# Kernel optimization log

Hardware: AMD Instinct MI355X
Metric: run time of the kernel (lower is better)

The kernel has to match this reference:

```python
import jax, jax.numpy as jnp
import numpy as np

B, T, D, R = 4, 1024, 512, 64
SLOTS = (1024, 256, 64)
K = 16


def _layernorm(x, g, b, eps=1e-5):
    m = jnp.mean(x, axis=-1, keepdims=True)
    v = jnp.mean(jnp.square(x - m), axis=-1, keepdims=True)
    return (x - m) * jax.lax.rsqrt(v + eps) * g + b


def _signed_softmax(x):
    # signed softmax over the slot axis: sign(x) * softmax(|x|)
    return jnp.sign(x) * jax.nn.softmax(jnp.abs(x), axis=-1)


def _transition_delta(src_val, src_state, dst_val, W, k, n_dst):
    # Low-rank bilinear routing: logits [B, Ns, Nd]
    q = jnp.einsum('bsd,dr->bsr', src_val, W[0])
    kk = jnp.einsum('bnd,dr->bnr', dst_val, W[1])
    logits = jnp.einsum('bsr,bnr->bsn', q, kk) / jnp.sqrt(jnp.float32(W.shape[-1]))
    v, idx = jax.lax.top_k(logits, k)                      # [B, Ns, k]
    w = jnp.sign(v) * jax.nn.softmax(jnp.abs(v), axis=-1)  # signed_abs_softmax over selected edges
    c = w * jax.nn.softplus(src_state)[:, :, None]         # state-weighted edge coefficients [B, Ns, k]
    d = src_val.shape[-1]
    edge_val = (c[..., None] * src_val[:, :, None, :]).reshape(src_val.shape[0], -1, d)
    idx_f = idx.reshape(idx.shape[0], -1)
    cf = c.reshape(c.shape[0], -1)

    def _scatter(i, ev, cc):
        dv = jnp.zeros((n_dst, d), src_val.dtype).at[i].add(ev)
        ds = jnp.zeros((n_dst,), src_val.dtype).at[i].add(cc)
        return ds, dv

    return jax.vmap(_scatter)(idx_f, edge_val, cf)


def _apply_delta(state, val, dstate, dval, g, b):
    # residual merge, then constrain: signed softmax state + LayerNorm values
    return _signed_softmax(state + dstate), _layernorm(val + dval, g, b)


def setup_inputs() -> dict:
    key = jax.random.key(0)
    ks = jax.random.split(key, 20)
    rn = lambda k, s, sc=1.0: jax.random.normal(k, s, jnp.float32) * sc
    return {
        'tok_val': rn(ks[0], (B, T, D)),
        'tok_state': rn(ks[1], (B, T)),
        'mem_state0': rn(ks[2], (B, SLOTS[0]), 0.02),
        'mem_val0': rn(ks[3], (B, SLOTS[0], D), 0.02),
        'mem_state1': rn(ks[4], (B, SLOTS[1]), 0.02),
        'mem_val1': rn(ks[5], (B, SLOTS[1], D), 0.02),
        'mem_state2': rn(ks[6], (B, SLOTS[2]), 0.02),
        'mem_val2': rn(ks[7], (B, SLOTS[2], D), 0.02),
        'write_route': rn(ks[8], (1, 2, D, R), 0.05),
        'prop_route': rn(ks[9], (3, 2, D, R), 0.05),
        'level_route': rn(ks[10], (2, 2, D, R), 0.05),
        'skip_route': rn(ks[11], (2, 2, D, R), 0.05),
        'skip_gates': jnp.full((2,), -1.5, jnp.float32),
        'ln_gamma': jnp.ones((3, D), jnp.float32),
        'ln_beta': jnp.zeros((3, D), jnp.float32),
        'read_route': rn(ks[12], (3, 2, D, R), 0.05),
        'read_proj': rn(ks[13], (3, D, D), 0.02),
        'read_gates': jnp.zeros((3,), jnp.float32),
        'topk': K,
    }


def reference(tok_val, tok_state, mem_state0, mem_val0, mem_state1, mem_val1,
              mem_state2, mem_val2, write_route, prop_route, level_route,
              skip_route, skip_gates, ln_gamma, ln_beta, read_route, read_proj,
              read_gates, topk):
    k = int(topk)
    S0, S1, S2 = mem_state0.shape[1], mem_state1.shape[1], mem_state2.shape[1]

    # --- level 0: token write + pairwise propagation ---
    ds, dv = _transition_delta(tok_val, tok_state, mem_val0, write_route[0], min(k, S0), S0)
    s0, v0 = _apply_delta(mem_state0, mem_val0, ds, dv, ln_gamma[0], ln_beta[0])
    ds, dv = _transition_delta(v0, s0, v0, prop_route[0], min(k, S0), S0)
    s0, v0 = _apply_delta(s0, v0, ds, dv, ln_gamma[0], ln_beta[0])

    # --- level 1: transition from level 0, gated skip from tokens, propagation ---
    ds, dv = _transition_delta(v0, s0, mem_val1, level_route[0], min(k, S1), S1)
    s1, v1 = _apply_delta(mem_state1, mem_val1, ds, dv, ln_gamma[1], ln_beta[1])
    g = jax.nn.sigmoid(skip_gates[0])
    ds, dv = _transition_delta(tok_val, tok_state, v1, skip_route[0], min(k, S1), S1)
    s1, v1 = _apply_delta(s1, v1, g * ds, g * dv, ln_gamma[1], ln_beta[1])
    ds, dv = _transition_delta(v1, s1, v1, prop_route[1], min(k, S1), S1)
    s1, v1 = _apply_delta(s1, v1, ds, dv, ln_gamma[1], ln_beta[1])

    # --- level 2: transition from level 1, gated skip from level 0, propagation ---
    ds, dv = _transition_delta(v1, s1, mem_val2, level_route[1], min(k, S2), S2)
    s2, v2 = _apply_delta(mem_state2, mem_val2, ds, dv, ln_gamma[2], ln_beta[2])
    g = jax.nn.sigmoid(skip_gates[1])
    ds, dv = _transition_delta(v0, s0, v2, skip_route[1], min(k, S2), S2)
    s2, v2 = _apply_delta(s2, v2, g * ds, g * dv, ln_gamma[2], ln_beta[2])
    ds, dv = _transition_delta(v2, s2, v2, prop_route[2], min(k, S2), S2)
    s2, v2 = _apply_delta(s2, v2, ds, dv, ln_gamma[2], ln_beta[2])

    # --- read: tokens attend over each memory level, gated projected residual ---
    out = tok_val
    for l, mv in enumerate((v0, v1, v2)):
        q = jnp.einsum('btd,dr->btr', tok_val, read_route[l, 0])
        kk = jnp.einsum('bnd,dr->bnr', mv, read_route[l, 1])
        logits = jnp.einsum('btr,bnr->btn', q, kk) / jnp.sqrt(jnp.float32(R))
        attn = jax.nn.softmax(logits, axis=-1)
        r = jnp.einsum('btn,bnd->btd', attn, mv)
        out = out + jax.nn.sigmoid(read_gates[l]) * jnp.einsum('btd,de->bte', r, read_proj[l])
    return out
```

## Files before the change

kernel.cpp:

```cpp
#include <hip/hip_runtime.h>
#include <math.h>

typedef __attribute__((ext_vector_type(8))) short short8;
typedef __attribute__((ext_vector_type(4))) float floatx4;

static __device__ __forceinline__ short f2bf(float f) {
    union { float f; unsigned u; } c; c.f = f;
    unsigned r = c.u + 0x7FFF + ((c.u >> 16) & 1);
    return (short)(r >> 16);
}

__launch_bounds__(256)
__global__ void gemm_f32_nt_kernel(const float* __restrict__ A, const float* __restrict__ B,
                                   float* __restrict__ C, int M, int N, int K,
                                   long sA, long sB, long sC, float alpha)
{
    __shared__ float As[32][68];
    __shared__ float Bs[32][68];
    const float* Ab = A + (long)blockIdx.z * sA;
    const float* Bb = B + (long)blockIdx.z * sB;
    float* Cb = C + (long)blockIdx.z * sC;
    int m0 = blockIdx.x * 64, n0 = blockIdx.y * 64;
    int t = threadIdx.x;
    int tx = t & 15, ty = t >> 4;
    float acc[4][4] = {};

    for (int k0 = 0; k0 < K; k0 += 32) {
        {
            int m = t >> 3;
            int kk = (t & 7) * 4;
#pragma unroll
            for (int h = 0; h < 2; ++h) {
                float4 v = *(const float4*)&Ab[(long)(m0 + m + 32 * h) * K + k0 + kk];
                As[kk + 0][m + 32 * h] = v.x; As[kk + 1][m + 32 * h] = v.y;
                As[kk + 2][m + 32 * h] = v.z; As[kk + 3][m + 32 * h] = v.w;
            }
        }
        {
            int n = t >> 3;
            int kk = (t & 7) * 4;
#pragma unroll
            for (int h = 0; h < 2; ++h) {
                float4 v = *(const float4*)&Bb[(long)(n0 + n + 32 * h) * K + k0 + kk];
                Bs[kk + 0][n + 32 * h] = v.x; Bs[kk + 1][n + 32 * h] = v.y;
                Bs[kk + 2][n + 32 * h] = v.z; Bs[kk + 3][n + 32 * h] = v.w;
            }
        }
        __syncthreads();
#pragma unroll 4
        for (int k = 0; k < 32; ++k) {
            float4 a = *(const float4*)&As[k][ty * 4];
            float4 b = *(const float4*)&Bs[k][tx * 4];
            float av[4] = { a.x, a.y, a.z, a.w };
            float bv[4] = { b.x, b.y, b.z, b.w };
#pragma unroll
            for (int i = 0; i < 4; ++i)
#pragma unroll
                for (int j = 0; j < 4; ++j) acc[i][j] += av[i] * bv[j];
        }
        __syncthreads();
    }
#pragma unroll
    for (int i = 0; i < 4; ++i) {
        float4 r;
        r.x = alpha * acc[i][0]; r.y = alpha * acc[i][1];
        r.z = alpha * acc[i][2]; r.w = alpha * acc[i][3];
        *(float4*)&Cb[(long)(m0 + ty * 4 + i) * N + n0 + tx * 4] = r;
    }
}

__launch_bounds__(256)
__global__ void proj_splitk_kernel(const float* __restrict__ Aq, const float* __restrict__ Ak,
                                   const float* __restrict__ Wq, const float* __restrict__ Wk,
                                   float* __restrict__ part,
                                   int Mq, int Mk, long sAq, long sAk, int Bn)
{
    __shared__ float As[32][68];
    __shared__ float Bs[32][68];
    int mqT = Mq >> 6;
    int xt = blockIdx.x, s = blockIdx.y, b = blockIdx.z;
    const float* A; const float* W; int row0, orow;
    if (xt < mqT) { A = Aq + (long)b * sAq; W = Wq; row0 = xt * 64; orow = row0; }
    else { A = Ak + (long)b * sAk; W = Wk; row0 = (xt - mqT) * 64; orow = Mq + row0; }
    int t = threadIdx.x, tx = t & 15, ty = t >> 4;
    float acc[4][4] = {};
    int kbase = s * 64;

    for (int k0 = kbase; k0 < kbase + 64; k0 += 32) {
        {
            int m = t >> 3;
            int kk = (t & 7) * 4;
#pragma unroll
            for (int h = 0; h < 2; ++h) {
                float4 v = *(const float4*)&A[(long)(row0 + m + 32 * h) * 512 + k0 + kk];
                As[kk + 0][m + 32 * h] = v.x; As[kk + 1][m + 32 * h] = v.y;
                As[kk + 2][m + 32 * h] = v.z; As[kk + 3][m + 32 * h] = v.w;
            }
        }
        {
            int kk = t >> 3;
            int nn = (t & 7) * 8;
            float4 v0 = *(const float4*)&W[(long)(k0 + kk) * 64 + nn];
            float4 v1 = *(const float4*)&W[(long)(k0 + kk) * 64 + nn + 4];
            *(float4*)&Bs[kk][nn] = v0;
            *(float4*)&Bs[kk][nn + 4] = v1;
        }
        __syncthreads();
#pragma unroll 4
        for (int k = 0; k < 32; ++k) {
            float4 a = *(const float4*)&As[k][ty * 4];
            float4 b2 = *(const float4*)&Bs[k][tx * 4];
            float av[4] = { a.x, a.y, a.z, a.w };
            float bv[4] = { b2.x, b2.y, b2.z, b2.w };
#pragma unroll
            for (int i = 0; i < 4; ++i)
#pragma unroll
                for (int j = 0; j < 4; ++j) acc[i][j] += av[i] * bv[j];
        }
        __syncthreads();
    }
    long base = ((long)(s * Bn + b) * (Mq + Mk) + orow) * 64;
#pragma unroll
    for (int i = 0; i < 4; ++i)
        *(float4*)&part[base + (long)(ty * 4 + i) * 64 + tx * 4] =
            make_float4(acc[i][0], acc[i][1], acc[i][2], acc[i][3]);
}

__launch_bounds__(256)
__global__ void proj_reduce_kernel(const float* __restrict__ part,
                                   float* __restrict__ qout, float* __restrict__ kout,
                                   int Mq, int Mk, int Bn)
{
    int idx = blockIdx.x * 256 + threadIdx.x;
    int size4b = (Mq + Mk) * 16;
    int total4 = Bn * size4b;
    if (idx >= total4) return;
    const float4* p4 = (const float4*)part;
    long stride4 = (long)total4;
    float4 s = p4[idx];
#pragma unroll
    for (int ss = 1; ss < 8; ++ss) {
        float4 v = p4[ss * stride4 + idx];
        s.x += v.x; s.y += v.y; s.z += v.z; s.w += v.w;
    }
    int b = idx / size4b;
    int rem = idx - b * size4b;
    int r = rem >> 4;
    int c4 = rem & 15;
    if (r < Mq) ((float4*)qout)[((long)b * Mq + r) * 16 + c4] = s;
    else        ((float4*)kout)[((long)b * Mk + (r - Mq)) * 16 + c4] = s;
}

__launch_bounds__(256)
__global__ void gemm_mfma_kernel(const float* __restrict__ A, const unsigned short* __restrict__ Bt,
                                 float* __restrict__ C, int M, int N, int K,
                                 long sA, long sBt, long sC,
                                 float alpha, const float* __restrict__ gate, int gateIdx,
                                 float beta, const float* __restrict__ initC)
{
    __shared__ short As[2048];
    __shared__ short Bs[2048];
    const float* Ab = A + (long)blockIdx.z * sA;
    const unsigned short* Bb = Bt + (long)blockIdx.z * sBt;
    float* Cb = C + (long)blockIdx.z * sC;
    const float* Ib = initC ? initC + (long)blockIdx.z * sC : nullptr;
    int m0 = blockIdx.x * 64, n0 = blockIdx.y * 64;
    int t = threadIdx.x, wave = t >> 6, lane = t & 63;
    int sr = wave * 16 + (lane & 15);
    int sk = (lane >> 4) * 8;
    floatx4 acc[4] = {};

    for (int k0 = 0; k0 < K; k0 += 32) {
        const float* ap = &Ab[(long)(m0 + sr) * K + k0 + sk];
        float4 f0 = *(const float4*)ap;
        float4 f1 = *(const float4*)(ap + 4);
        short8 av;
        av[0] = f2bf(f0.x); av[1] = f2bf(f0.y); av[2] = f2bf(f0.z); av[3] = f2bf(f0.w);
        av[4] = f2bf(f1.x); av[5] = f2bf(f1.y); av[6] = f2bf(f1.z); av[7] = f2bf(f1.w);
        short8 bv = *(const short8*)&Bb[(long)(n0 + sr) * K + k0 + sk];
        ((short8*)As)[t] = av;
        ((short8*)Bs)[t] = bv;
        __syncthreads();
        short8 bf = ((short8*)Bs)[wave * 64 + lane];
#pragma unroll
        for (int mt = 0; mt < 4; ++mt) {
            short8 af = ((short8*)As)[mt * 64 + lane];
            acc[mt] = __builtin_amdgcn_mfma_f32_16x16x32_bf16(af, bf, acc[mt], 0, 0, 0);
        }
        __syncthreads();
    }
    float a = alpha;
    if (gate) a *= 1.f / (1.f + expf(-gate[gateIdx]));
    int col = n0 + wave * 16 + (lane & 15);
#pragma unroll
    for (int mt = 0; mt < 4; ++mt) {
#pragma unroll
        for (int r = 0; r < 4; ++r) {
            int row = m0 + mt * 16 + (lane >> 4) * 4 + r;
            long off = (long)row * N + col;
            float v = a * acc[mt][r];
            if (Ib) v += Ib[off];
            else if (beta != 0.f) v += Cb[off];
            Cb[off] = v;
        }
    }
}

__global__ void transpose_bf16_kernel(const float* __restrict__ in, unsigned short* __restrict__ out,
                                      int Rr, int Cc, long sIn, long sOut)
{
    __shared__ float tile[32][33];
    const float* I = in + (long)blockIdx.z * sIn;
    unsigned short* O = out + (long)blockIdx.z * sOut;
    int c0 = blockIdx.x * 32, r0 = blockIdx.y * 32;
    int tx = threadIdx.x, ty = threadIdx.y;
#pragma unroll
    for (int i = 0; i < 32; i += 8)
        tile[ty + i][tx] = I[(long)(r0 + ty + i) * Cc + c0 + tx];
    __syncthreads();
#pragma unroll
    for (int i = 0; i < 32; i += 8)
        O[(long)(c0 + ty + i) * Rr + r0 + tx] = (unsigned short)f2bf(tile[tx][ty + i]);
}

template<int CNT>
__launch_bounds__(256)
__global__ void topk_coeff_kernel(const float* __restrict__ logits,
                                  const float* __restrict__ state,
                                  int* __restrict__ idx_out, float* __restrict__ c_out,
                                  int* __restrict__ cnt, int nsLog, int Nd)
{
    int wave = threadIdx.x >> 6, lane = threadIdx.x & 63;
    long row = (long)blockIdx.x * 4 + wave;
    const float* L = logits + row * Nd;
    float vreg[CNT];
    if (CNT >= 4) {
#pragma unroll
        for (int q = 0; q < CNT / 4; ++q) {
            float4 v = *(const float4*)&L[lane * CNT + q * 4];
            vreg[q * 4 + 0] = v.x; vreg[q * 4 + 1] = v.y;
            vreg[q * 4 + 2] = v.z; vreg[q * 4 + 3] = v.w;
        }
    } else {
#pragma unroll
        for (int tt = 0; tt < CNT; ++tt) vreg[tt] = L[lane * CNT + tt];
    }

    float m = 0.f, sum = 0.f;
    float myv = 0.f; int myi = 0;
#pragma unroll
    for (int it = 0; it < 16; ++it) {
        float best = -INFINITY; int bidx = 0x7fffffff;
#pragma unroll
        for (int tt = 0; tt < CNT; ++tt) {
            if (vreg[tt] > best) { best = vreg[tt]; bidx = lane * CNT + tt; }
        }
#pragma unroll
        for (int off = 32; off; off >>= 1) {
            float ov = __shfl_down(best, off);
            int   oi = __shfl_down(bidx, off);
            if (ov > best || (ov == best && oi < bidx)) { best = ov; bidx = oi; }
        }
        best = __shfl(best, 0);
        bidx = __shfl(bidx, 0);
        if (it == lane) { myv = best; myi = bidx; }
        float ab = fabsf(best);
        float nm = fmaxf(m, ab);
        sum = sum * expf(m - nm) + expf(ab - nm);
        m = nm;
#pragma unroll
        for (int tt = 0; tt < CNT; ++tt)
            if (lane * CNT + tt == bidx) vreg[tt] = -INFINITY;
    }
    if (lane < 16) {
        float st = state[row];
        float sp = fmaxf(st, 0.f) + log1pf(expf(-fabsf(st)));
        float sgn = (myv > 0.f) ? 1.f : ((myv < 0.f) ? -1.f : 0.f);
        float w = expf(fabsf(myv) - m) / sum;
        c_out[row * 16 + lane] = sgn * w * sp;
        idx_out[row * 16 + lane] = myi;
        int b = (int)(row >> nsLog);
        atomicAdd(&cnt[b * Nd + myi], 1);
    }
}

__launch_bounds__(256)
__global__ void scan_kernel(int* __restrict__ cnt, int* __restrict__ offs, int N)
{
    __shared__ int sums[256];
    int t = threadIdx.x;
    int chunk = N >> 8;
    int base = t * chunk;
    int lc[16];
    int s = 0;
    for (int i = 0; i < chunk; ++i) { lc[i] = cnt[base + i]; s += lc[i]; }
    sums[t] = s;
    __syncthreads();
    for (int off = 1; off < 256; off <<= 1) {
        int v = (t >= off) ? sums[t - off] : 0;
        __syncthreads();
        sums[t] += v;
        __syncthreads();
    }
    int run = sums[t] - s;
    for (int i = 0; i < chunk; ++i) {
        offs[base + i] = run;
        run += lc[i];
        cnt[base + i] = 0;
    }
    if (t == 255) offs[N] = run;
}

__launch_bounds__(256)
__global__ void fill_edges_kernel(const int* __restrict__ idx, const int* __restrict__ offs,
                                  int* __restrict__ cursor, int* __restrict__ elist,
                                  int nsShift, int Nd, int E)
{
    int e = blockIdx.x * 256 + threadIdx.x;
    if (e >= E) return;
    int b = e >> nsShift;
    int d = b * Nd + idx[e];
    int pos = offs[d] + atomicAdd(&cursor[d], 1);
    elist[pos] = e;
}

#define ECHUNK 512
__launch_bounds__(256)
__global__ void gather_ln_kernel(const float* __restrict__ src_val, const float* __restrict__ c,
                                 const int* __restrict__ elist, const int* __restrict__ offs,
                                 const float* __restrict__ v_in, float* __restrict__ v_out,
                                 float* __restrict__ ds, int* __restrict__ cursor,
                                 const float* __restrict__ gamma, const float* __restrict__ beta,
                                 const float* __restrict__ gatePtr, int gateIdx, int nsShift)
{
    __shared__ float sc[ECHUNK];
    __shared__ int   srow[ECHUNK];
    __shared__ float part[4][512];
    __shared__ float pcs[4];
    __shared__ float red[4];
    long row = blockIdx.x;
    int t = threadIdx.x, w = t >> 6, lane = t & 63;
    int e0 = offs[row], e1 = offs[row + 1];
    int mask = (1 << nsShift) - 1;
    int cb = lane * 8;
    float a[8] = {};
    float cs = 0.f;
    float gate = 1.f;
    if (gatePtr) gate = 1.f / (1.f + expf(-gatePtr[gateIdx]));

    for (int cstart = e0; cstart < e1; cstart += ECHUNK) {
        int cnt = min(e1 - cstart, ECHUNK);
        for (int i = t; i < cnt; i += 256) {
            int e = elist[cstart + i];
            sc[i] = c[e];
            int b = e >> nsShift;
            int s = (e & mask) >> 4;
            srow[i] = (b << (nsShift - 4)) + s;
        }
        __syncthreads();
        int j = w;
        for (; j + 12 < cnt; j += 16) {
            float c0 = sc[j], c1 = sc[j + 4], c2 = sc[j + 8], c3 = sc[j + 12];
            const float* p0 = src_val + ((long)srow[j]      << 9) + cb;
            const float* p1 = src_val + ((long)srow[j + 4]  << 9) + cb;
            const float* p2 = src_val + ((long)srow[j + 8]  << 9) + cb;
            const float* p3 = src_val + ((long)srow[j + 12] << 9) + cb;
            float4 x00 = *(const float4*)p0,       x01 = *(const float4*)(p0 + 4);
            float4 x10 = *(const float4*)p1,       x11 = *(const float4*)(p1 + 4);
            float4 x20 = *(const float4*)p2,       x21 = *(const float4*)(p2 + 4);
            float4 x30 = *(const float4*)p3,       x31 = *(const float4*)(p3 + 4);
            a[0] += c0 * x00.x + c1 * x10.x + c2 * x20.x + c3 * x30.x;
            a[1] += c0 * x00.y + c1 * x10.y + c2 * x20.y + c3 * x30.y;
            a[2] += c0 * x00.z + c1 * x10.z + c2 * x20.z + c3 * x30.z;
            a[3] += c0 * x00.w + c1 * x10.w + c2 * x20.w + c3 * x30.w;
            a[4] += c0 * x01.x + c1 * x11.x + c2 * x21.x + c3 * x31.x;
            a[5] += c0 * x01.y + c1 * x11.y + c2 * x21.y + c3 * x31.y;
            a[6] += c0 * x01.z + c1 * x11.z + c2 * x21.z + c3 * x31.z;
            a[7] += c0 * x01.w + c1 * x11.w + c2 * x21.w + c3 * x31.w;
            cs += c0 + c1 + c2 + c3;
        }
        for (; j < cnt; j += 4) {
            float cv = sc[j];
            const float* p = src_val + ((long)srow[j] << 9) + cb;
            float4 x0 = *(const float4*)p, x1 = *(const float4*)(p + 4);
            a[0] += cv * x0.x; a[1] += cv * x0.y; a[2] += cv * x0.z; a[3] += cv * x0.w;
            a[4] += cv * x1.x; a[5] += cv * x1.y; a[6] += cv * x1.z; a[7] += cv * x1.w;
            cs += cv;
        }
        __syncthreads();
    }
#pragma unroll
    for (int i = 0; i < 8; ++i) part[w][cb + i] = a[i];
    if (lane == 0) pcs[w] = cs;
    __syncthreads();
    float r0 = part[0][t] + part[1][t] + part[2][t] + part[3][t];
    float r1 = part[0][t + 256] + part[1][t + 256] + part[2][t + 256] + part[3][t + 256];
    if (t == 0) { ds[row] = pcs[0] + pcs[1] + pcs[2] + pcs[3]; cursor[row] = 0; }

    const float* vi = v_in + (row << 9);
    float x0 = vi[t]       + gate * r0;
    float x1 = vi[t + 256] + gate * r1;
    float s = x0 + x1;
    for (int off = 32; off; off >>= 1) s += __shfl_down(s, off);
    if ((t & 63) == 0) red[t >> 6] = s;
    __syncthreads();
    float mean = (red[0] + red[1] + red[2] + red[3]) * (1.f / 512.f);
    float d0 = x0 - mean, d1 = x1 - mean;
    float ss = d0 * d0 + d1 * d1;
    for (int off = 32; off; off >>= 1) ss += __shfl_down(ss, off);
    __syncthreads();
    if ((t & 63) == 0) red[t >> 6] = ss;
    __syncthreads();
    float var = (red[0] + red[1] + red[2] + red[3]) * (1.f / 512.f);
    float rstd = rsqrtf(var + 1e-5f);
    float* vo = v_out + (row << 9);
    vo[t]       = d0 * rstd * gamma[t]       + beta[t];
    vo[t + 256] = d1 * rstd * gamma[t + 256] + beta[t + 256];
}

__launch_bounds__(256)
__global__ void apply_state_kernel(const float* __restrict__ s_in, const float* __restrict__ ds,
                                   float* __restrict__ s_out, int Nd,
                                   const float* __restrict__ gatePtr, int gateIdx)
{
    __shared__ float sh[1024];
    __shared__ float red[4];
    int b = blockIdx.x, t = threadIdx.x;
    float gate = 1.f;
    if (gatePtr) gate = 1.f / (1.f + expf(-gatePtr[gateIdx]));
    float lmax = 0.f;
    for (int i = t; i < Nd; i += 256) {
        float x = s_in[b * Nd + i] + gate * ds[b * Nd + i];
        sh[i] = x;
        lmax = fmaxf(lmax, fabsf(x));
    }
    for (int off = 32; off; off >>= 1) lmax = fmaxf(lmax, __shfl_down(lmax, off));
    if ((t & 63) == 0) red[t >> 6] = lmax;
    __syncthreads();
    float bmax = fmaxf(fmaxf(red[0], red[1]), fmaxf(red[2], red[3]));
    float lsum = 0.f;
    for (int i = t; i < Nd; i += 256) lsum += expf(fabsf(sh[i]) - bmax);
    for (int off = 32; off; off >>= 1) lsum += __shfl_down(lsum, off);
    __syncthreads();
    if ((t & 63) == 0) red[t >> 6] = lsum;
    __syncthreads();
    float inv = 1.f / (red[0] + red[1] + red[2] + red[3]);
    for (int i = t; i < Nd; i += 256) {
        float x = sh[i];
        float sgn = (x > 0.f) ? 1.f : ((x < 0.f) ? -1.f : 0.f);
        s_out[b * Nd + i] = sgn * expf(fabsf(x) - bmax) * inv;
    }
}

__launch_bounds__(256)
__global__ void softmax_rows_kernel(float* __restrict__ logits, int Nd)
{
    __shared__ float red[4];
    long row = blockIdx.x;
    int t = threadIdx.x;
    float* L = logits + row * (long)Nd;
    float lmax = -INFINITY;
    for (int i = t; i < Nd; i += 256) lmax = fmaxf(lmax, L[i]);
    for (int off = 32; off; off >>= 1) lmax = fmaxf(lmax, __shfl_down(lmax, off));
    if ((t & 63) == 0) red[t >> 6] = lmax;
    __syncthreads();
    float bmax = fmaxf(fmaxf(red[0], red[1]), fmaxf(red[2], red[3]));
    float lsum = 0.f;
    for (int i = t; i < Nd; i += 256) lsum += expf(L[i] - bmax);
    for (int off = 32; off; off >>= 1) lsum += __shfl_down(lsum, off);
    __syncthreads();
    if ((t & 63) == 0) red[t >> 6] = lsum;
    __syncthreads();
    float inv = 1.f / (red[0] + red[1] + red[2] + red[3]);
    for (int i = t; i < Nd; i += 256) L[i] = expf(L[i] - bmax) * inv;
}

extern "C" void kernel_launch(void* const* d_in, const int* in_sizes, int n_in,
                              void* d_out, int out_size, void* d_ws, size_t ws_size,
                              hipStream_t stream)
{
    const int Bn = 4, T = 1024, D = 512, R = 64;
    const int S0 = 1024, S1 = 256, S2 = 64;
    const long RT = (long)D * R;

    const float* tok_val    = (const float*)d_in[0];
    const float* tok_state  = (const float*)d_in[1];
    const float* mem_state0 = (const float*)d_in[2];
    const float* mem_val0   = (const float*)d_in[3];
    const float* mem_state1 = (const float*)d_in[4];
    const float* mem_val1   = (const float*)d_in[5];
    const float* mem_state2 = (const float*)d_in[6];
    const float* mem_val2   = (const float*)d_in[7];
    const float* write_route= (const float*)d_in[8];
    const float* prop_route = (const float*)d_in[9];
    const float* level_route= (const float*)d_in[10];
    const float* skip_route = (const float*)d_in[11];
    const float* skip_gates = (const float*)d_in[12];
    const float* ln_gamma   = (const float*)d_in[13];
    const float* ln_beta    = (const float*)d_in[14];
    const float* read_route = (const float*)d_in[15];
    const float* read_proj  = (const float*)d_in[16];
    const float* read_gates = (const float*)d_in[17];
    float* out = (float*)d_out;

    float* p = (float*)d_ws;
    float* v0  = p; p += (long)Bn * S0 * D;
    float* v0b = p; p += (long)Bn * S0 * D;
    float* s0  = p; p += Bn * S0;
    float* v1  = p; p += (long)Bn * S1 * D;
    float* v1b = p; p += (long)Bn * S1 * D;
    float* s1  = p; p += Bn * S1;
    float* v2  = p; p += (long)Bn * S2 * D;
    float* v2b = p; p += (long)Bn * S2 * D;
    float* s2  = p; p += Bn * S2;
    float* qb  = p; p += (long)Bn * T * R;
    float* kb  = p; p += (long)Bn * S0 * R;
    float* lb  = p; p += (long)Bn * T * S0;
    float* cbuf= p; p += (long)Bn * T * 16;
    int*   ib  = (int*)p; p += (long)Bn * T * 16;
    float* dsb = p; p += Bn * S0;
    float* rb  = p; p += (long)Bn * T * D;
    int* cntb  = (int*)p; p += Bn * S0;
    int* curb  = (int*)p; p += Bn * S0;
    int* offsb = (int*)p; p += Bn * S0 + 1;
    int* elistb= (int*)p; p += (long)Bn * T * 16;
    unsigned short* projT = (unsigned short*)p; p += (3 * (long)D * D) / 2 + 4;
    unsigned short* mvT   = (unsigned short*)p; p += ((long)Bn * D * S0) / 2 + 4;
    float* partb = p; p += 8L * Bn * (T + S0) * R;

    auto proj = [&](const float* Aq, const float* Ak, const float* Wq, const float* Wk,
                    int Mq, int Mk, long sAq, long sAk, float* qout, float* kout) {
        proj_splitk_kernel<<<dim3((Mq + Mk) / 64, 8, Bn), 256, 0, stream>>>(
            Aq, Ak, Wq, Wk, partb, Mq, Mk, sAq, sAk, Bn);
        int total4 = Bn * (Mq + Mk) * 16;
        proj_reduce_kernel<<<(total4 + 255) / 256, 256, 0, stream>>>(
            partb, qout, kout, Mq, Mk, Bn);
    };

    hipMemsetAsync(cntb, 0, (size_t)2 * Bn * S0 * sizeof(int), stream);

    auto trans = [&](const float* sv, const float* ss, const float* dval,
                     const float* W, int Ns, int Nd,
                     const float* v_in, float* v_out, const float* sin, float* sout,
                     int lvl, const float* gptr, int gidx) {
        proj(sv, dval, W, W + RT, Ns, Nd, (long)Ns * D, (long)Nd * D, qb, kb);
        gemm_f32_nt_kernel<<<dim3(Ns / 64, Nd / 64, Bn), 256, 0, stream>>>(
            qb, kb, lb, Ns, Nd, R, (long)Ns * R, (long)Nd * R, (long)Ns * Nd, 0.125f);
        int nsLog = 31 - __builtin_clz((unsigned)Ns);
        int nsShift = nsLog + 4;
        int rowBlocks = Bn * Ns / 4;
        if (Nd == 1024)
            topk_coeff_kernel<16><<<rowBlocks, 256, 0, stream>>>(lb, ss, ib, cbuf, cntb, nsLog, Nd);
        else if (Nd == 256)
            topk_coeff_kernel<4><<<rowBlocks, 256, 0, stream>>>(lb, ss, ib, cbuf, cntb, nsLog, Nd);
        else
            topk_coeff_kernel<1><<<rowBlocks, 256, 0, stream>>>(lb, ss, ib, cbuf, cntb, nsLog, Nd);
        int E = Bn * Ns * 16;
        scan_kernel<<<1, 256, 0, stream>>>(cntb, offsb, Bn * Nd);
        fill_edges_kernel<<<(E + 255) / 256, 256, 0, stream>>>(ib, offsb, curb, elistb,
                                                               nsShift, Nd, E);
        gather_ln_kernel<<<Bn * Nd, 256, 0, stream>>>(sv, cbuf, elistb, offsb,
                                                      v_in, v_out, dsb, curb,
                                                      ln_gamma + lvl * D, ln_beta + lvl * D,
                                                      gptr, gidx, nsShift);
        apply_state_kernel<<<Bn, 256, 0, stream>>>(sin, dsb, sout, Nd, gptr, gidx);
    };

    trans(tok_val, tok_state, mem_val0, write_route, T, S0,
          mem_val0, v0, mem_state0, s0, 0, nullptr, 0);
    trans(v0, s0, v0, prop_route + 0 * 2 * RT, S0, S0,
          v0, v0b, s0, s0, 0, nullptr, 0);

    trans(v0b, s0, mem_val1, level_route + 0 * 2 * RT, S0, S1,
          mem_val1, v1, mem_state1, s1, 1, nullptr, 0);
    trans(tok_val, tok_state, v1, skip_route + 0 * 2 * RT, T, S1,
          v1, v1, s1, s1, 1, skip_gates, 0);
    trans(v1, s1, v1, prop_route + 1 * 2 * RT, S1, S1,
          v1, v1b, s1, s1, 1, nullptr, 0);

    trans(v1b, s1, mem_val2, level_route + 1 * 2 * RT, S1, S2,
          mem_val2, v2, mem_state2, s2, 2, nullptr, 0);
    trans(v0b, s0, v2, skip_route + 1 * 2 * RT, S0, S2,
          v2, v2, s2, s2, 2, skip_gates, 1);
    trans(v2, s2, v2, prop_route + 2 * 2 * RT, S2, S2,
          v2, v2b, s2, s2, 2, nullptr, 0);

    transpose_bf16_kernel<<<dim3(D / 32, D / 32, 3), dim3(32, 8), 0, stream>>>(
        read_proj, projT, D, D, (long)D * D, (long)D * D);
    const float* mvs[3] = { v0b, v1b, v2b };
    const int nds[3] = { S0, S1, S2 };
    for (int l = 0; l < 3; ++l) {
        const float* mv = mvs[l];
        int Nd = nds[l];
        proj(tok_val, mv, read_route + (long)l * 2 * RT, read_route + (long)l * 2 * RT + RT,
             T, Nd, (long)T * D, (long)Nd * D, qb, kb);
        gemm_f32_nt_kernel<<<dim3(T / 64, Nd / 64, Bn), 256, 0, stream>>>(
            qb, kb, lb, T, Nd, R, (long)T * R, (long)Nd * R, (long)T * Nd, 0.125f);
        softmax_rows_kernel<<<Bn * T, 256, 0, stream>>>(lb, Nd);
        transpose_bf16_kernel<<<dim3(D / 32, Nd / 32, Bn), dim3(32, 8), 0, stream>>>(
            mv, mvT, Nd, D, (long)Nd * D, (long)D * Nd);
        gemm_mfma_kernel<<<dim3(T / 64, D / 64, Bn), 256, 0, stream>>>(
            lb, mvT, rb, T, D, Nd, (long)T * Nd, (long)D * Nd, (long)T * D,
            1.f, nullptr, 0, 0.f, nullptr);
        gemm_mfma_kernel<<<dim3(T / 64, D / 64, Bn), 256, 0, stream>>>(
            rb, projT + (long)l * D * D, out, T, D, D,
            (long)T * D, 0, (long)T * D, 1.f, read_gates, l,
            1.f, (l == 0) ? tok_val : nullptr);
    }
}
```

Baseline: 925.0 us.

## Batch read-side projections and transposes, fuse state update into gather-LN kernel

Generalizes the split-K projection kernel to take a descriptor of up to six segments. All six read-path Q/K projections now run in one launch plus one reduce, and the reduce writes a contiguous layout instead of scattering into separate q/k buffers. The three memory-value transposes are merged into one launch. The state scatter-add and signed softmax now run as extra blocks of the gather-LN kernel using shared-memory atomics, which removes the separate apply-state launch and the global ds buffer. The goal is fewer kernel launches and less tail time, at the cost of branchy segment lookup and atomic accumulation whose order is nondeterministic.

Result: slower. 1.014 ms (+9.6%).

```diff
diff --git a/kernel.cpp b/kernel.cpp
--- a/kernel.cpp
+++ b/kernel.cpp
@@ -69,19 +69,27 @@
     }
 }
 
-__launch_bounds__(256)
-__global__ void proj_splitk_kernel(const float* __restrict__ Aq, const float* __restrict__ Ak,
-                                   const float* __restrict__ Wq, const float* __restrict__ Wk,
-                                   float* __restrict__ part,
-                                   int Mq, int Mk, long sAq, long sAk, int Bn)
+struct ProjDesc {
+    const float* A[6];
+    const float* W[6];
+    long  sA[6];
+    int   tileOff[7];
+    int   rowOff[6];
+    int   Mtot;
+};
+
+__launch_bounds__(256)
+__global__ void proj_splitk_kernel(ProjDesc d, float* __restrict__ part, int Bn)
 {
     __shared__ float As[32][68];
     __shared__ float Bs[32][68];
-    int mqT = Mq >> 6;
     int xt = blockIdx.x, s = blockIdx.y, b = blockIdx.z;
-    const float* A; const float* W; int row0, orow;
-    if (xt < mqT) { A = Aq + (long)b * sAq; W = Wq; row0 = xt * 64; orow = row0; }
-    else { A = Ak + (long)b * sAk; W = Wk; row0 = (xt - mqT) * 64; orow = Mq + row0; }
+    int seg = 0;
+    while (xt >= d.tileOff[seg + 1]) ++seg;
+    int row0 = (xt - d.tileOff[seg]) * 64;
+    const float* A = d.A[seg] + (long)b * d.sA[seg];
+    const float* W = d.W[seg];
+    int orow = d.rowOff[seg] + row0;
     int t = threadIdx.x, tx = t & 15, ty = t >> 4;
     float acc[4][4] = {};
     int kbase = s * 64;
@@ -119,7 +127,7 @@
         }
         __syncthreads();
     }
-    long base = ((long)(s * Bn + b) * (Mq + Mk) + orow) * 64;
+    long base = ((long)(s * Bn + b) * d.Mtot + orow) * 64;
 #pragma unroll
     for (int i = 0; i < 4; ++i)
         *(float4*)&part[base + (long)(ty * 4 + i) * 64 + tx * 4] =
@@ -127,28 +135,19 @@
 }
 
 __launch_bounds__(256)
-__global__ void proj_reduce_kernel(const float* __restrict__ part,
-                                   float* __restrict__ qout, float* __restrict__ kout,
-                                   int Mq, int Mk, int Bn)
+__global__ void proj_reduce_kernel(const float* __restrict__ part, float* __restrict__ outp,
+                                   int total4)
 {
     int idx = blockIdx.x * 256 + threadIdx.x;
-    int size4b = (Mq + Mk) * 16;
-    int total4 = Bn * size4b;
     if (idx >= total4) return;
     const float4* p4 = (const float4*)part;
-    long stride4 = (long)total4;
     float4 s = p4[idx];
 #pragma unroll
     for (int ss = 1; ss < 8; ++ss) {
-        float4 v = p4[ss * stride4 + idx];
+        float4 v = p4[(long)ss * total4 + idx];
         s.x += v.x; s.y += v.y; s.z += v.z; s.w += v.w;
     }
-    int b = idx / size4b;
-    int rem = idx - b * size4b;
-    int r = rem >> 4;
-    int c4 = rem & 15;
-    if (r < Mq) ((float4*)qout)[((long)b * Mq + r) * 16 + c4] = s;
-    else        ((float4*)kout)[((long)b * Mk + (r - Mq)) * 16 + c4] = s;
+    ((float4*)outp)[idx] = s;
 }
 
 __launch_bounds__(256)
@@ -223,6 +222,30 @@
         O[(long)(c0 + ty + i) * Rr + r0 + tx] = (unsigned short)f2bf(tile[tx][ty + i]);
 }
 
+__global__ void transpose_mv_kernel(const float* __restrict__ mv0, const float* __restrict__ mv1,
+                                    const float* __restrict__ mv2,
+                                    unsigned short* __restrict__ o0, unsigned short* __restrict__ o1,
+                                    unsigned short* __restrict__ o2)
+{
+    __shared__ float tile[32][33];
+    int yt = blockIdx.y;
+    const float* in; unsigned short* out; int Nd, r0t;
+    if (yt < 32)      { in = mv0; out = o0; Nd = 1024; r0t = yt; }
+    else if (yt < 40) { in = mv1; out = o1; Nd = 256;  r0t = yt - 32; }
+    else              { in = mv2; out = o2; Nd = 64;   r0t = yt - 40; }
+    const float* I = in + (long)blockIdx.z * Nd * 512;
+    unsigned short* O = out + (long)blockIdx.z * 512 * Nd;
+    int c0 = blockIdx.x * 32, r0 = r0t * 32;
+    int tx = threadIdx.x, ty = threadIdx.y;
+#pragma unroll
+    for (int i = 0; i < 32; i += 8)
+        tile[ty + i][tx] = I[(long)(r0 + ty + i) * 512 + c0 + tx];
+    __syncthreads();
+#pragma unroll
+    for (int i = 0; i < 32; i += 8)
+        O[(long)(c0 + ty + i) * Nd + r0 + tx] = (unsigned short)f2bf(tile[tx][ty + i]);
+}
+
 template<int CNT>
 __launch_bounds__(256)
 __global__ void topk_coeff_kernel(const float* __restrict__ logits,
@@ -326,129 +349,130 @@
 
 #define ECHUNK 512
 __launch_bounds__(256)
-__global__ void gather_ln_kernel(const float* __restrict__ src_val, const float* __restrict__ c,
-                                 const int* __restrict__ elist, const int* __restrict__ offs,
-                                 const float* __restrict__ v_in, float* __restrict__ v_out,
-                                 float* __restrict__ ds, int* __restrict__ cursor,
-                                 const float* __restrict__ gamma, const float* __restrict__ beta,
-                                 const float* __restrict__ gatePtr, int gateIdx, int nsShift)
+__global__ void gather_ln_state_kernel(const float* __restrict__ src_val, const float* __restrict__ c,
+                                       const int* __restrict__ eidx, const int* __restrict__ elist,
+                                       const int* __restrict__ offs,
+                                       const float* __restrict__ v_in, float* __restrict__ v_out,
+                                       const float* __restrict__ s_in, float* __restrict__ s_out,
+                                       int* __restrict__ cursor,
+                                       const float* __restrict__ gamma, const float* __restrict__ beta,
+                                       const float* __restrict__ gatePtr, int gateIdx,
+                                       int nsShift, int Nd, int Ns, int Bn)
 {
     __shared__ float sc[ECHUNK];
     __shared__ int   srow[ECHUNK];
     __shared__ float part[4][512];
-    __shared__ float pcs[4];
     __shared__ float red[4];
-    long row = blockIdx.x;
-    int t = threadIdx.x, w = t >> 6, lane = t & 63;
-    int e0 = offs[row], e1 = offs[row + 1];
-    int mask = (1 << nsShift) - 1;
-    int cb = lane * 8;
-    float a[8] = {};
-    float cs = 0.f;
+    int t = threadIdx.x;
     float gate = 1.f;
     if (gatePtr) gate = 1.f / (1.f + expf(-gatePtr[gateIdx]));
-
-    for (int cstart = e0; cstart < e1; cstart += ECHUNK) {
-        int cnt = min(e1 - cstart, ECHUNK);
-        for (int i = t; i < cnt; i += 256) {
-            int e = elist[cstart + i];
-            sc[i] = c[e];
-            int b = e >> nsShift;
-            int s = (e & mask) >> 4;
-            srow[i] = (b << (nsShift - 4)) + s;
-        }
-        __syncthreads();
-        int j = w;
-        for (; j + 12 < cnt; j += 16) {
-            float c0 = sc[j], c1 = sc[j + 4], c2 = sc[j + 8], c3 = sc[j + 12];
-            const float* p0 = src_val + ((long)srow[j]      << 9) + cb;
-            const float* p1 = src_val + ((long)srow[j + 4]  << 9) + cb;
-            const float* p2 = src_val + ((long)srow[j + 8]  << 9) + cb;
-            const float* p3 = src_val + ((long)srow[j + 12] << 9) + cb;
-            float4 x00 = *(const float4*)p0,       x01 = *(const float4*)(p0 + 4);
-            float4 x10 = *(const float4*)p1,       x11 = *(const float4*)(p1 + 4);
-            float4 x20 = *(const float4*)p2,       x21 = *(const float4*)(p2 + 4);
-            float4 x30 = *(const float4*)p3,       x31 = *(const float4*)(p3 + 4);
-            a[0] += c0 * x00.x + c1 * x10.x + c2 * x20.x + c3 * x30.x;
-            a[1] += c0 * x00.y + c1 * x10.y + c2 * x20.y + c3 * x30.y;
-            a[2] += c0 * x00.z + c1 * x10.z + c2 * x20.z + c3 * x30.z;
-            a[3] += c0 * x00.w + c1 * x10.w + c2 * x20.w + c3 * x30.w;
-            a[4] += c0 * x01.x + c1 * x11.x + c2 * x21.x + c3 * x31.x;
-            a[5] += c0 * x01.y + c1 * x11.y + c2 * x21.y + c3 * x31.y;
-            a[6] += c0 * x01.z + c1 * x11.z + c2 * x21.z + c3 * x31.z;
-            a[7] += c0 * x01.w + c1 * x11.w + c2 * x21.w + c3 * x31.w;
-            cs += c0 + c1 + c2 + c3;
-        }
-        for (; j < cnt; j += 4) {
-            float cv = sc[j];
-            const float* p = src_val + ((long)srow[j] << 9) + cb;
-            float4 x0 = *(const float4*)p, x1 = *(const float4*)(p + 4);
-            a[0] += cv * x0.x; a[1] += cv * x0.y; a[2] += cv * x0.z; a[3] += cv * x0.w;
-            a[4] += cv * x1.x; a[5] += cv * x1.y; a[6] += cv * x1.z; a[7] += cv * x1.w;
-            cs += cv;
-        }
-        __syncthreads();
-    }
-#pragma unroll
-    for (int i = 0; i < 8; ++i) part[w][cb + i] = a[i];
-    if (lane == 0) pcs[w] = cs;
-    __syncthreads();
-    float r0 = part[0][t] + part[1][t] + part[2][t] + part[3][t];
-    float r1 = part[0][t + 256] + part[1][t + 256] + part[2][t + 256] + part[3][t + 256];
-    if (t == 0) { ds[row] = pcs[0] + pcs[1] + pcs[2] + pcs[3]; cursor[row] = 0; }
-
-    const float* vi = v_in + (row << 9);
-    float x0 = vi[t]       + gate * r0;
-    float x1 = vi[t + 256] + gate * r1;
-    float s = x0 + x1;
-    for (int off = 32; off; off >>= 1) s += __shfl_down(s, off);
-    if ((t & 63) == 0) red[t >> 6] = s;
-    __syncthreads();
-    float mean = (red[0] + red[1] + red[2] + red[3]) * (1.f / 512.f);
-    float d0 = x0 - mean, d1 = x1 - mean;
-    float ss = d0 * d0 + d1 * d1;
-    for (int off = 32; off; off >>= 1) ss += __shfl_down(ss, off);
-    __syncthreads();
-    if ((t & 63) == 0) red[t >> 6] = ss;
-    __syncthreads();
-    float var = (red[0] + red[1] + red[2] + red[3]) * (1.f / 512.f);
-    float rstd = rsqrtf(var + 1e-5f);
-    float* vo = v_out + (row << 9);
-    vo[t]       = d0 * rstd * gamma[t]       + beta[t];
-    vo[t + 256] = d1 * rstd * gamma[t + 256] + beta[t + 256];
-}
-
-__launch_bounds__(256)
-__global__ void apply_state_kernel(const float* __restrict__ s_in, const float* __restrict__ ds,
-                                   float* __restrict__ s_out, int Nd,
-                                   const float* __restrict__ gatePtr, int gateIdx)
-{
-    __shared__ float sh[1024];
-    __shared__ float red[4];
-    int b = blockIdx.x, t = threadIdx.x;
-    float gate = 1.f;
-    if (gatePtr) gate = 1.f / (1.f + expf(-gatePtr[gateIdx]));
-    float lmax = 0.f;
-    for (int i = t; i < Nd; i += 256) {
-        float x = s_in[b * Nd + i] + gate * ds[b * Nd + i];
-        sh[i] = x;
-        lmax = fmaxf(lmax, fabsf(x));
-    }
-    for (int off = 32; off; off >>= 1) lmax = fmaxf(lmax, __shfl_down(lmax, off));
-    if ((t & 63) == 0) red[t >> 6] = lmax;
-    __syncthreads();
-    float bmax = fmaxf(fmaxf(red[0], red[1]), fmaxf(red[2], red[3]));
-    float lsum = 0.f;
-    for (int i = t; i < Nd; i += 256) lsum += expf(fabsf(sh[i]) - bmax);
-    for (int off = 32; off; off >>= 1) lsum += __shfl_down(lsum, off);
-    __syncthreads();
-    if ((t & 63) == 0) red[t >> 6] = lsum;
-    __syncthreads();
-    float inv = 1.f / (red[0] + red[1] + red[2] + red[3]);
-    for (int i = t; i < Nd; i += 256) {
-        float x = sh[i];
-        float sgn = (x > 0.f) ? 1.f : ((x < 0.f) ? -1.f : 0.f);
-        s_out[b * Nd + i] = sgn * expf(fabsf(x) - bmax) * inv;
+    int nLN = gridDim.x - Bn;
+
+    if ((int)blockIdx.x < nLN) {
+        long row = blockIdx.x;
+        int w = t >> 6, lane = t & 63;
+        int e0 = offs[row], e1 = offs[row + 1];
+        int mask = (1 << nsShift) - 1;
+        int cb = lane * 8;
+        float a[8] = {};
+
+        for (int cstart = e0; cstart < e1; cstart += ECHUNK) {
+            int cnt = min(e1 - cstart, ECHUNK);
+            for (int i = t; i < cnt; i += 256) {
+                int e = elist[cstart + i];
+                sc[i] = c[e];
+                int b = e >> nsShift;
+                int s = (e & mask) >> 4;
+                srow[i] = (b << (nsShift - 4)) + s;
+            }
+            __syncthreads();
+            int j = w;
+            for (; j + 12 < cnt; j += 16) {
+                float c0 = sc[j], c1 = sc[j + 4], c2 = sc[j + 8], c3 = sc[j + 12];
+                const float* p0 = src_val + ((long)srow[j]      << 9) + cb;
+                const float* p1 = src_val + ((long)srow[j + 4]  << 9) + cb;
+                const float* p2 = src_val + ((long)srow[j + 8]  << 9) + cb;
+                const float* p3 = src_val + ((long)srow[j + 12] << 9) + cb;
+                float4 x00 = *(const float4*)p0,       x01 = *(const float4*)(p0 + 4);
+                float4 x10 = *(const float4*)p1,       x11 = *(const float4*)(p1 + 4);
+                float4 x20 = *(const float4*)p2,       x21 = *(const float4*)(p2 + 4);
+                float4 x30 = *(const float4*)p3,       x31 = *(const float4*)(p3 + 4);
+                a[0] += c0 * x00.x + c1 * x10.x + c2 * x20.x + c3 * x30.x;
+                a[1] += c0 * x00.y + c1 * x10.y + c2 * x20.y + c3 * x30.y;
+                a[2] += c0 * x00.z + c1 * x10.z + c2 * x20.z + c3 * x30.z;
+                a[3] += c0 * x00.w + c1 * x10.w + c2 * x20.w + c3 * x30.w;
+                a[4] += c0 * x01.x + c1 * x11.x + c2 * x21.x + c3 * x31.x;
+                a[5] += c0 * x01.y + c1 * x11.y + c2 * x21.y + c3 * x31.y;
+                a[6] += c0 * x01.z + c1 * x11.z + c2 * x21.z + c3 * x31.z;
+                a[7] += c0 * x01.w + c1 * x11.w + c2 * x21.w + c3 * x31.w;
+            }
+            for (; j < cnt; j += 4) {
+                float cv = sc[j];
+                const float* p = src_val + ((long)srow[j] << 9) + cb;
+                float4 x0 = *(const float4*)p, x1 = *(const float4*)(p + 4);
+                a[0] += cv * x0.x; a[1] += cv * x0.y; a[2] += cv * x0.z; a[3] += cv * x0.w;
+                a[4] += cv * x1.x; a[5] += cv * x1.y; a[6] += cv * x1.z; a[7] += cv * x1.w;
+            }
+            __syncthreads();
+        }
+#pragma unroll
+        for (int i = 0; i < 8; ++i) part[w][cb + i] = a[i];
+        __syncthreads();
+        float r0 = part[0][t] + part[1][t] + part[2][t] + part[3][t];
+        float r1 = part[0][t + 256] + part[1][t + 256] + part[2][t + 256] + part[3][t + 256];
+        if (t == 0) cursor[row] = 0;
+
+        const float* vi = v_in + (row << 9);
+        float x0 = vi[t]       + gate * r0;
+        float x1 = vi[t + 256] + gate * r1;
+        float s = x0 + x1;
+        for (int off = 32; off; off >>= 1) s += __shfl_down(s, off);
+        if ((t & 63) == 0) red[t >> 6] = s;
+        __syncthreads();
+        float mean = (red[0] + red[1] + red[2] + red[3]) * (1.f / 512.f);
+        float d0 = x0 - mean, d1 = x1 - mean;
+        float ss = d0 * d0 + d1 * d1;
+        for (int off = 32; off; off >>= 1) ss += __shfl_down(ss, off);
+        __syncthreads();
+        if ((t & 63) == 0) red[t >> 6] = ss;
+        __syncthreads();
+        float var = (red[0] + red[1] + red[2] + red[3]) * (1.f / 512.f);
+        float rstd = rsqrtf(var + 1e-5f);
+        float* vo = v_out + (row << 9);
+        vo[t]       = d0 * rstd * gamma[t]       + beta[t];
+        vo[t + 256] = d1 * rstd * gamma[t + 256] + beta[t + 256];
+    } else {
+        __shared__ float dsl[1024];
+        int b = (int)blockIdx.x - nLN;
+        for (int i = t; i < Nd; i += 256) dsl[i] = 0.f;
+        __syncthreads();
+        int Eb = Ns * 16;
+        int ebase = b * Eb;
+        for (int e = t; e < Eb; e += 256)
+            atomicAdd(&dsl[eidx[ebase + e]], c[ebase + e]);
+        __syncthreads();
+        float lmax = 0.f;
+        for (int i = t; i < Nd; i += 256) {
+            float x = s_in[b * Nd + i] + gate * dsl[i];
+            dsl[i] = x;
+            lmax = fmaxf(lmax, fabsf(x));
+        }
+        for (int off = 32; off; off >>= 1) lmax = fmaxf(lmax, __shfl_down(lmax, off));
+        if ((t & 63) == 0) red[t >> 6] = lmax;
+        __syncthreads();
+        float bmax = fmaxf(fmaxf(red[0], red[1]), fmaxf(red[2], red[3]));
+        float lsum = 0.f;
+        for (int i = t; i < Nd; i += 256) lsum += expf(fabsf(dsl[i]) - bmax);
+        for (int off = 32; off; off >>= 1) lsum += __shfl_down(lsum, off);
+        __syncthreads();
+        if ((t & 63) == 0) red[t >> 6] = lsum;
+        __syncthreads();
+        float inv = 1.f / (red[0] + red[1] + red[2] + red[3]);
+        for (int i = t; i < Nd; i += 256) {
+            float x = dsl[i];
+            float sgn = (x > 0.f) ? 1.f : ((x < 0.f) ? -1.f : 0.f);
+            s_out[b * Nd + i] = sgn * expf(fabsf(x) - bmax) * inv;
+        }
     }
 }
 
@@ -482,6 +506,7 @@
     const int Bn = 4, T = 1024, D = 512, R = 64;
     const int S0 = 1024, S1 = 256, S2 = 64;
     const long RT = (long)D * R;
+    const int MR = 3 * T + S0 + S1 + S2;
 
     const float* tok_val    = (const float*)d_in[0];
     const float* tok_state  = (const float*)d_in[1];
@@ -513,29 +538,21 @@
     float* v2  = p; p += (long)Bn * S2 * D;
     float* v2b = p; p += (long)Bn * S2 * D;
     float* s2  = p; p += Bn * S2;
-    float* qb  = p; p += (long)Bn * T * R;
-    float* kb  = p; p += (long)Bn * S0 * R;
+    float* qk  = p; p += (long)Bn * (T + S0) * R;
+    float* rqk = p; p += (long)Bn * MR * R;
     float* lb  = p; p += (long)Bn * T * S0;
     float* cbuf= p; p += (long)Bn * T * 16;
     int*   ib  = (int*)p; p += (long)Bn * T * 16;
-    float* dsb = p; p += Bn * S0;
     float* rb  = p; p += (long)Bn * T * D;
     int* cntb  = (int*)p; p += Bn * S0;
     int* curb  = (int*)p; p += Bn * S0;
     int* offsb = (int*)p; p += Bn * S0 + 1;
     int* elistb= (int*)p; p += (long)Bn * T * 16;
     unsigned short* projT = (unsigned short*)p; p += (3 * (long)D * D) / 2 + 4;
-    unsigned short* mvT   = (unsigned short*)p; p += ((long)Bn * D * S0) / 2 + 4;
-    float* partb = p; p += 8L * Bn * (T + S0) * R;
-
-    auto proj = [&](const float* Aq, const float* Ak, const float* Wq, const float* Wk,
-                    int Mq, int Mk, long sAq, long sAk, float* qout, float* kout) {
-        proj_splitk_kernel<<<dim3((Mq + Mk) / 64, 8, Bn), 256, 0, stream>>>(
-            Aq, Ak, Wq, Wk, partb, Mq, Mk, sAq, sAk, Bn);
-        int total4 = Bn * (Mq + Mk) * 16;
-        proj_reduce_kernel<<<(total4 + 255) / 256, 256, 0, stream>>>(
-            partb, qout, kout, Mq, Mk, Bn);
-    };
+    unsigned short* mvT0  = (unsigned short*)p; p += ((long)Bn * D * S0) / 2 + 4;
+    unsigned short* mvT1  = (unsigned short*)p; p += ((long)Bn * D * S1) / 2 + 4;
+    unsigned short* mvT2  = (unsigned short*)p; p += ((long)Bn * D * S2) / 2 + 4;
+    float* partb = p; p += 8L * Bn * MR * R;
 
     hipMemsetAsync(cntb, 0, (size_t)2 * Bn * S0 * sizeof(int), stream);
 
@@ -543,9 +560,20 @@
                      const float* W, int Ns, int Nd,
                      const float* v_in, float* v_out, const float* sin, float* sout,
                      int lvl, const float* gptr, int gidx) {
-        proj(sv, dval, W, W + RT, Ns, Nd, (long)Ns * D, (long)Nd * D, qb, kb);
+        int Mtot = Ns + Nd;
+        ProjDesc d = {};
+        d.A[0] = sv;   d.W[0] = W;      d.sA[0] = (long)Ns * D; d.rowOff[0] = 0;
+        d.A[1] = dval; d.W[1] = W + RT; d.sA[1] = (long)Nd * D; d.rowOff[1] = Ns;
+        int tot = Mtot / 64;
+        d.tileOff[0] = 0; d.tileOff[1] = Ns / 64;
+        for (int i = 2; i <= 6; ++i) d.tileOff[i] = tot;
+        d.Mtot = Mtot;
+        proj_splitk_kernel<<<dim3(tot, 8, Bn), 256, 0, stream>>>(d, partb, Bn);
+        int total4 = Bn * Mtot * 16;
+        proj_reduce_kernel<<<(total4 + 255) / 256, 256, 0, stream>>>(partb, qk, total4);
         gemm_f32_nt_kernel<<<dim3(Ns / 64, Nd / 64, Bn), 256, 0, stream>>>(
-            qb, kb, lb, Ns, Nd, R, (long)Ns * R, (long)Nd * R, (long)Ns * Nd, 0.125f);
+            qk, qk + (long)Ns * R, lb, Ns, Nd, R,
+            (long)Mtot * R, (long)Mtot * R, (long)Ns * Nd, 0.125f);
         int nsLog = 31 - __builtin_clz((unsigned)Ns);
         int nsShift = nsLog + 4;
         int rowBlocks = Bn * Ns / 4;
@@ -559,11 +587,9 @@
         scan_kernel<<<1, 256, 0, stream>>>(cntb, offsb, Bn * Nd);
         fill_edges_kernel<<<(E + 255) / 256, 256, 0, stream>>>(ib, offsb, curb, elistb,
                                                                nsShift, Nd, E);
-        gather_ln_kernel<<<Bn * Nd, 256, 0, stream>>>(sv, cbuf, elistb, offsb,
-                                                      v_in, v_out, dsb, curb,
-                                                      ln_gamma + lvl * D, ln_beta + lvl * D,
-                                                      gptr, gidx, nsShift);
-        apply_state_kernel<<<Bn, 256, 0, stream>>>(sin, dsb, sout, Nd, gptr, gidx);
+        gather_ln_state_kernel<<<Bn * Nd + Bn, 256, 0, stream>>>(
+            sv, cbuf, ib, elistb, offsb, v_in, v_out, sin, sout, curb,
+            ln_gamma + lvl * D, ln_beta + lvl * D, gptr, gidx, nsShift, Nd, Ns, Bn);
     };
 
     trans(tok_val, tok_state, mem_val0, write_route, T, S0,
@@ -587,20 +613,43 @@
 
     transpose_bf16_kernel<<<dim3(D / 32, D / 32, 3), dim3(32, 8), 0, stream>>>(
         read_proj, projT, D, D, (long)D * D, (long)D * D);
-    const float* mvs[3] = { v0b, v1b, v2b };
+    transpose_mv_kernel<<<dim3(D / 32, (S0 + S1 + S2) / 32, Bn), dim3(32, 8), 0, stream>>>(
+        v0b, v1b, v2b, mvT0, mvT1, mvT2);
+
+    {
+        ProjDesc d = {};
+        const float* mvs[3] = { v0b, v1b, v2b };
+        const int nds[3] = { S0, S1, S2 };
+        int tiles = 0, roff = 0;
+        for (int l = 0; l < 3; ++l) {
+            d.A[l] = tok_val; d.W[l] = read_route + (long)l * 2 * RT;
+            d.sA[l] = (long)T * D; d.rowOff[l] = roff;
+            d.tileOff[l] = tiles; tiles += T / 64; roff += T;
+        }
+        for (int l = 0; l < 3; ++l) {
+            d.A[3 + l] = mvs[l]; d.W[3 + l] = read_route + (long)l * 2 * RT + RT;
+            d.sA[3 + l] = (long)nds[l] * D; d.rowOff[3 + l] = roff;
+            d.tileOff[3 + l] = tiles; tiles += nds[l] / 64; roff += nds[l];
+        }
+        d.tileOff[6] = tiles;
+        d.Mtot = MR;
+        proj_splitk_kernel<<<dim3(tiles, 8, Bn), 256, 0, stream>>>(d, partb, Bn);
+        int total4 = Bn * MR * 16;
+        proj_reduce_kernel<<<(total4 + 255) / 256, 256, 0, stream>>>(partb, rqk, total4);
+    }
+
+    const unsigned short* mvTs[3] = { mvT0, mvT1, mvT2 };
     const int nds[3] = { S0, S1, S2 };
+    int koff = 3 * T;
     for (int l = 0; l < 3; ++l) {
-        const float* mv = mvs[l];
         int Nd = nds[l];
-        proj(tok_val, mv, read_route + (long)l * 2 * RT, read_route + (long)l * 2 * RT + RT,
-             T, Nd, (long)T * D, (long)Nd * D, qb, kb);
         gemm_f32_nt_kernel<<<dim3(T / 64, Nd / 64, Bn), 256, 0, stream>>>(
-            qb, kb, lb, T, Nd, R, (long)T * R, (long)Nd * R, (long)T * Nd, 0.125f);
+            rqk + (long)l * T * R, rqk + (long)koff * R, lb, T, Nd, R,
+            (long)MR * R, (long)MR * R, (long)T * Nd, 0.125f);
+        koff += Nd;
         softmax_rows_kernel<<<Bn * T, 256, 0, stream>>>(lb, Nd);
-        transpose_bf16_kernel<<<dim3(D / 32, Nd / 32, Bn), dim3(32, 8), 0, stream>>>(
-            mv, mvT, Nd, D, (long)Nd * D, (long)D * Nd);
         gemm_mfma_kernel<<<dim3(T / 64, D / 64, Bn), 256, 0, stream>>>(
-            lb, mvT, rb, T, D, Nd, (long)T * Nd, (long)D * Nd, (long)T * D,
+            lb, mvTs[l], rb, T, D, Nd, (long)T * Nd, (long)D * Nd, (long)T * D,
             1.f, nullptr, 0, 0.f, nullptr);
         gemm_mfma_kernel<<<dim3(T / 64, D / 64, Bn), 256, 0, stream>>>(
             rb, projT + (long)l * D * D, out, T, D, D,
```
